# Performance work log

Hardware: AMD Instinct MI355X
Metric: run time of the kernel (lower is better)

Reference implementation:

```python
import jax, jax.numpy as jnp
import numpy as np

NEG_INF = jnp.float32(-(2.0**32) + 1.0)


def squash(z):
    # z: [B, k_max, out_units]
    sq_norm = jnp.sum(jnp.square(z), axis=-1, keepdims=True)
    scale = sq_norm / (1.0 + sq_norm) / jnp.sqrt(sq_norm + 1e-8)
    return scale * z


def setup_inputs() -> dict:
    key = jax.random.key(0)
    k1, k2, k3, k4 = jax.random.split(key, 4)
    B, L, D_IN, D_OUT, K = 1024, 200, 256, 256, 8
    behavior_embeddings = jax.random.normal(k1, (B, L, D_IN), dtype=jnp.float32)
    seq_len = jax.random.randint(k2, (B, 1), 1, L + 1, dtype=jnp.int32)
    routing_logits = jax.random.normal(k3, (1, K, L), dtype=jnp.float32)  # init_std=1.0
    bilinear_mapping_matrix = jax.random.normal(k4, (D_IN, D_OUT), dtype=jnp.float32)
    return {
        "behavior_embeddings": behavior_embeddings,
        "seq_len": seq_len,
        "routing_logits": routing_logits,
        "bilinear_mapping_matrix": bilinear_mapping_matrix,
    }


def reference(behavior_embeddings, seq_len, routing_logits, bilinear_mapping_matrix):
    ITERATION_TIMES = 3
    B, L, _ = behavior_embeddings.shape
    K = routing_logits.shape[1]

    # mask: [B, 1, L] broadcastable to [B, K, L] (same seq_len for every capsule)
    mask = jnp.arange(L)[None, None, :] < seq_len[:, :, None]

    # bilinear map is loop-invariant: [B, L, out_units]
    mapped = jnp.einsum("ble,eo->blo", behavior_embeddings, bilinear_mapping_matrix)

    logits = routing_logits  # [1, K, L]
    interest_capsules = None
    for _ in range(ITERATION_TIMES):
        logits_pad = jnp.where(mask, jnp.broadcast_to(logits, (B, K, L)), NEG_INF)
        weight = jax.nn.softmax(logits_pad, axis=-1)          # [B, K, L]
        Z = jnp.einsum("bkl,blo->bko", weight, mapped)         # [B, K, out]
        interest_capsules = squash(Z)                          # [B, K, out]
        # delta: sum over batch of capsules @ mapped^T -> [1, K, L]
        delta = jnp.einsum("bko,blo->kl", interest_capsules, mapped)[None]
        logits = logits + delta  # emulates assign_add on non-trainable B

    return interest_capsules.reshape(-1, K, interest_capsules.shape[-1])
```

## Files before the change

kernel.cpp:

```cpp
#include <hip/hip_runtime.h>
#include <cstdint>
#include <cstddef>

#define B_    1024
#define L_    200
#define DIN_  256
#define DOUT_ 256
#define K_    8
#define M_    (B_ * L_)

typedef __attribute__((ext_vector_type(8))) short bf16x8;
typedef __attribute__((ext_vector_type(4))) float f32x4;

__device__ __forceinline__ float bf2f(unsigned short u) {
  union { unsigned int i; float f; } w; w.i = ((unsigned int)u) << 16; return w.f;
}
__device__ __forceinline__ unsigned short f2bf(float f) {
  union { float f; unsigned int i; } w; w.f = f;
  unsigned int x = w.i;
  return (unsigned short)((x + 0x7fffu + ((x >> 16) & 1u)) >> 16);
}

__device__ __forceinline__ void gload_lds16(const unsigned short* g, unsigned short* l) {
  __builtin_amdgcn_global_load_lds(
      (const __attribute__((address_space(1))) void*)g,
      (__attribute__((address_space(3))) void*)l, 16, 0, 0);
}

__global__ __launch_bounds__(256)
void wt_prep(const float* __restrict__ W, const float* __restrict__ rlog,
             unsigned short* __restrict__ Wall, float* __restrict__ logitsW)
{
  const int k = blockIdx.x;
  const int n = threadIdx.x;
  const int gi = blockIdx.x * 256 + threadIdx.x;
  if (gi < K_ * L_) logitsW[gi] = rlog[gi];

  float x = W[k * DOUT_ + n];
  unsigned short h = f2bf(x);
  float r = x - bf2f(h);
  unsigned short m = f2bf(r);
  float r2 = r - bf2f(m);
  unsigned short l = f2bf(r2);
  const int k0b = k >> 5, quad = (k >> 3) & 3, j = k & 7;
  const int ntg = n >> 4, lr = n & 15;
  const int lane = quad * 16 + lr;
  Wall[(((size_t)k0b * 3 + 0) * 16 + ntg) * 512 + lane * 8 + j] = h;
  Wall[(((size_t)k0b * 3 + 1) * 16 + ntg) * 512 + lane * 8 + j] = m;
  Wall[(((size_t)k0b * 3 + 2) * 16 + ntg) * 512 + lane * 8 + j] = l;
}

__global__ __launch_bounds__(256, 3)
void gemm_mapped(const float* __restrict__ A,
                 const unsigned short* __restrict__ Wall,
                 float* __restrict__ C)
{
  const int t    = threadIdx.x;
  const int wave = t >> 6;
  const int lane = t & 63;
  const int quad = lane >> 4;
  const int lr   = lane & 15;
  const int m0   = blockIdx.x * 128 + wave * 32;
  const int nt0  = blockIdx.y * 8;

  __shared__ unsigned short Bs[2][24 * 512];

  f32x4 acc[2][8];
  #pragma unroll
  for (int mt = 0; mt < 2; ++mt)
    #pragma unroll
    for (int nt = 0; nt < 8; ++nt)
      acc[mt][nt] = (f32x4){0.f, 0.f, 0.f, 0.f};

  bf16x8 ah[2], am[2], al[2];
  float4 Af[2][2];

#define STAGE(K0B, BUF) do { \
    _Pragma("unroll") \
    for (int _i = 0; _i < 6; ++_i) { \
      const int _c   = wave * 6 + _i; \
      const int _s   = _c >> 3; \
      const int _ntl = _c & 7; \
      const unsigned short* _g = Wall + \
          ((((size_t)(K0B) * 3 + _s) * 16 + nt0 + _ntl) * 512) + lane * 8; \
      gload_lds16(_g, &Bs[BUF][_c * 512]); \
    } \
  } while (0)

  const float* ap0 = A + (size_t)(m0 + lr) * DIN_ + quad * 8;
  const float* ap1 = A + (size_t)(m0 + 16 + lr) * DIN_ + quad * 8;

  STAGE(0, 0);
  Af[0][0] = *(const float4*)(ap0);
  Af[0][1] = *(const float4*)(ap0 + 4);
  Af[1][0] = *(const float4*)(ap1);
  Af[1][1] = *(const float4*)(ap1 + 4);
  __syncthreads();

  for (int k0b = 0; k0b < 8; ++k0b) {
    const int cur = k0b & 1;
    if (k0b < 7) STAGE(k0b + 1, cur ^ 1);

    #pragma unroll
    for (int mt = 0; mt < 2; ++mt) {
      float xs[8] = {Af[mt][0].x, Af[mt][0].y, Af[mt][0].z, Af[mt][0].w,
                     Af[mt][1].x, Af[mt][1].y, Af[mt][1].z, Af[mt][1].w};
      #pragma unroll
      for (int j = 0; j < 8; ++j) {
        unsigned short h = f2bf(xs[j]);
        float r = xs[j] - bf2f(h);
        unsigned short mm = f2bf(r);
        float r2 = r - bf2f(mm);
        unsigned short ll = f2bf(r2);
        ah[mt][j] = (short)h; am[mt][j] = (short)mm; al[mt][j] = (short)ll;
      }
    }
    if (k0b < 7) {
      const int ko = (k0b + 1) * 32;
      Af[0][0] = *(const float4*)(ap0 + ko);
      Af[0][1] = *(const float4*)(ap0 + ko + 4);
      Af[1][0] = *(const float4*)(ap1 + ko);
      Af[1][1] = *(const float4*)(ap1 + ko + 4);
    }

#define GROUP(NT) do { \
    bf16x8 bh = *(const bf16x8*)&Bs[cur][(0 * 8 + (NT)) * 512 + lane * 8]; \
    bf16x8 bm = *(const bf16x8*)&Bs[cur][(1 * 8 + (NT)) * 512 + lane * 8]; \
    bf16x8 bl = *(const bf16x8*)&Bs[cur][(2 * 8 + (NT)) * 512 + lane * 8]; \
    f32x4 c0 = acc[0][NT], c1 = acc[1][NT]; \
    c0 = __builtin_amdgcn_mfma_f32_16x16x32_bf16(ah[0], bh, c0, 0, 0, 0); \
    c1 = __builtin_amdgcn_mfma_f32_16x16x32_bf16(ah[1], bh, c1, 0, 0, 0); \
    c0 = __builtin_amdgcn_mfma_f32_16x16x32_bf16(ah[0], bm, c0, 0, 0, 0); \
    c1 = __builtin_amdgcn_mfma_f32_16x16x32_bf16(ah[1], bm, c1, 0, 0, 0); \
    c0 = __builtin_amdgcn_mfma_f32_16x16x32_bf16(am[0], bh, c0, 0, 0, 0); \
    c1 = __builtin_amdgcn_mfma_f32_16x16x32_bf16(am[1], bh, c1, 0, 0, 0); \
    c0 = __builtin_amdgcn_mfma_f32_16x16x32_bf16(ah[0], bl, c0, 0, 0, 0); \
    c1 = __builtin_amdgcn_mfma_f32_16x16x32_bf16(ah[1], bl, c1, 0, 0, 0); \
    c0 = __builtin_amdgcn_mfma_f32_16x16x32_bf16(am[0], bm, c0, 0, 0, 0); \
    c1 = __builtin_amdgcn_mfma_f32_16x16x32_bf16(am[1], bm, c1, 0, 0, 0); \
    c0 = __builtin_amdgcn_mfma_f32_16x16x32_bf16(al[0], bh, c0, 0, 0, 0); \
    c1 = __builtin_amdgcn_mfma_f32_16x16x32_bf16(al[1], bh, c1, 0, 0, 0); \
    acc[0][NT] = c0; acc[1][NT] = c1; \
  } while (0)

    GROUP(0); GROUP(1); GROUP(2); GROUP(3);
    GROUP(4); GROUP(5); GROUP(6); GROUP(7);
#undef GROUP

    __syncthreads();
  }
#undef STAGE

  #pragma unroll
  for (int mt = 0; mt < 2; ++mt)
    #pragma unroll
    for (int nt = 0; nt < 8; ++nt)
      #pragma unroll
      for (int r = 0; r < 4; ++r) {
        int row = m0 + mt * 16 + quad * 4 + r;
        C[(size_t)row * DOUT_ + (nt0 + nt) * 16 + lr] = acc[mt][nt][r];
      }
}

__global__ __launch_bounds__(256)
void z_kernel(const float* __restrict__ mapped, const float* __restrict__ logits,
              const int* __restrict__ seq_len, float* __restrict__ caps)
{
  const int t    = threadIdx.x;
  const int lane = t & 63;
  const int wave = t >> 6;
  const int b    = blockIdx.x * 4 + wave;
  const int len  = seq_len[b];
  __shared__ float w[4][K_][204];

  #pragma unroll
  for (int k = 0; k < K_; ++k) {
    float v[4];
    float mx = -3.4028235e38f;
    #pragma unroll
    for (int i = 0; i < 4; ++i) {
      int l = lane + 64 * i;
      v[i] = (l < len) ? logits[k * L_ + l] : -3.4028235e38f;
      mx = fmaxf(mx, v[i]);
    }
    #pragma unroll
    for (int s = 1; s < 64; s <<= 1) mx = fmaxf(mx, __shfl_xor(mx, s, 64));
    float e[4]; float sum = 0.f;
    #pragma unroll
    for (int i = 0; i < 4; ++i) {
      int l = lane + 64 * i;
      e[i] = (l < len) ? __expf(v[i] - mx) : 0.f;
      sum += e[i];
    }
    #pragma unroll
    for (int s = 1; s < 64; s <<= 1) sum += __shfl_xor(sum, s, 64);
    float inv = 1.f / sum;
    #pragma unroll
    for (int i = 0; i < 4; ++i) {
      int l = lane + 64 * i;
      if (l < 204) w[wave][k][l] = e[i] * inv;
    }
  }

  f32x4 acc[K_];
  #pragma unroll
  for (int k = 0; k < K_; ++k) acc[k] = (f32x4){0.f, 0.f, 0.f, 0.f};
  const float* mp = mapped + (size_t)b * L_ * DOUT_ + lane * 4;
  const int lceil = (len + 3) & ~3;
  for (int l = 0; l < lceil; l += 4) {
    float4 m0 = *(const float4*)(mp + (size_t)(l + 0) * DOUT_);
    float4 m1 = *(const float4*)(mp + (size_t)(l + 1) * DOUT_);
    float4 m2 = *(const float4*)(mp + (size_t)(l + 2) * DOUT_);
    float4 m3 = *(const float4*)(mp + (size_t)(l + 3) * DOUT_);
    #pragma unroll
    for (int k = 0; k < K_; ++k) {
      float4 wv = *(const float4*)&w[wave][k][l];
      f32x4 c = acc[k];
      c.x += wv.x * m0.x + wv.y * m1.x + wv.z * m2.x + wv.w * m3.x;
      c.y += wv.x * m0.y + wv.y * m1.y + wv.z * m2.y + wv.w * m3.y;
      c.z += wv.x * m0.z + wv.y * m1.z + wv.z * m2.z + wv.w * m3.z;
      c.w += wv.x * m0.w + wv.y * m1.w + wv.z * m2.w + wv.w * m3.w;
      acc[k] = c;
    }
  }

  #pragma unroll
  for (int k = 0; k < K_; ++k) {
    float sq = acc[k].x * acc[k].x + acc[k].y * acc[k].y
             + acc[k].z * acc[k].z + acc[k].w * acc[k].w;
    #pragma unroll
    for (int s = 1; s < 64; s <<= 1) sq += __shfl_xor(sq, s, 64);
    float scale = sq / ((1.f + sq) * sqrtf(sq + 1e-8f));
    float4 o;
    o.x = scale * acc[k].x; o.y = scale * acc[k].y;
    o.z = scale * acc[k].z; o.w = scale * acc[k].w;
    *(float4*)&caps[((size_t)b * K_ + k) * DOUT_ + lane * 4] = o;
  }
}

__global__ __launch_bounds__(256)
void delta_kernel(const float* __restrict__ mapped, const float* __restrict__ caps,
                  float* __restrict__ partials)
{
  const int t    = threadIdx.x;
  const int lane = t & 63;
  const int wave = t >> 6;
  const int lc   = blockIdx.x % 13;
  const int bc   = blockIdx.x / 13;
  const int bsub = (wave >> 1) * 8;
  const int lsub = (wave & 1) * 8;
  const int l0   = lc * 16 + lsub;
  const int b0   = bc * 16 + bsub;
  const int o4   = lane * 4;

  float acc[K_][8];
  #pragma unroll
  for (int k = 0; k < K_; ++k)
    #pragma unroll
    for (int ll = 0; ll < 8; ++ll) acc[k][ll] = 0.f;

  for (int bi = 0; bi < 8; ++bi) {
    const int b = b0 + bi;
    const float* cp = caps + (size_t)b * (K_ * DOUT_) + o4;
    const float* mp = mapped + ((size_t)b * L_ + l0) * DOUT_ + o4;
    float4 cv[K_], mv[8];
    #pragma unroll
    for (int k = 0; k < K_; ++k) cv[k] = *(const float4*)(cp + (size_t)k * DOUT_);
    #pragma unroll
    for (int ll = 0; ll < 8; ++ll) {
      mv[ll] = (l0 + ll < L_) ? *(const float4*)(mp + (size_t)ll * DOUT_)
                              : make_float4(0.f, 0.f, 0.f, 0.f);
    }
    #pragma unroll
    for (int k = 0; k < K_; ++k)
      #pragma unroll
      for (int ll = 0; ll < 8; ++ll)
        acc[k][ll] += cv[k].x * mv[ll].x + cv[k].y * mv[ll].y
                    + cv[k].z * mv[ll].z + cv[k].w * mv[ll].w;
  }

  float out = 0.f;
  #pragma unroll
  for (int k = 0; k < K_; ++k)
    #pragma unroll
    for (int ll = 0; ll < 8; ++ll) {
      float v = acc[k][ll];
      v += __shfl_xor(v, 1, 64);
      v += __shfl_xor(v, 2, 64);
      v += __shfl_xor(v, 4, 64);
      v += __shfl_xor(v, 8, 64);
      v += __shfl_xor(v, 16, 64);
      v += __shfl_xor(v, 32, 64);
      if (lane == k * 8 + ll) out = v;
    }
  __shared__ float red[4][64];
  red[wave][lane] = out;
  __syncthreads();
  if (wave < 2) {
    float v = red[wave][lane] + red[wave + 2][lane];
    const int k  = lane >> 3;
    const int ll = lane & 7;
    const int gl = lc * 16 + wave * 8 + ll;
    if (gl < L_) partials[((size_t)bc * K_ + k) * L_ + gl] = v;
  }
}

__global__ __launch_bounds__(256)
void reduce_kernel(const float* __restrict__ partials, float* __restrict__ logits)
{
  int i = blockIdx.x * 256 + threadIdx.x;
  if (i < K_ * L_) {
    float s = 0.f;
    #pragma unroll 4
    for (int bc = 0; bc < 64; ++bc) s += partials[bc * (K_ * L_) + i];
    logits[i] += s;
  }
}

extern "C" void kernel_launch(void* const* d_in, const int* in_sizes, int n_in,
                              void* d_out, int out_size, void* d_ws, size_t ws_size,
                              hipStream_t stream)
{
  const float* behav = (const float*)d_in[0];
  const int*   slen  = (const int*)d_in[1];
  const float* rlog  = (const float*)d_in[2];
  const float* W     = (const float*)d_in[3];
  float* caps = (float*)d_out;

  char* ws = (char*)d_ws;
  float* logitsW  = (float*)ws;
  float* partials = (float*)(ws + 8192);
  unsigned short* Wall = (unsigned short*)(ws + 458752);
  float* mapped   = (float*)(ws + (1 << 20));

  wt_prep<<<dim3(256), 256, 0, stream>>>(W, rlog, Wall, logitsW);
  gemm_mapped<<<dim3(1600, 2), 256, 0, stream>>>(behav, Wall, mapped);
  for (int it = 0; it < 3; ++it) {
    z_kernel<<<dim3(B_ / 4), 256, 0, stream>>>(mapped, logitsW, slen, caps);
    if (it < 2) {
      delta_kernel<<<dim3(13 * 64), 256, 0, stream>>>(mapped, caps, partials);
      reduce_kernel<<<dim3(7), 256, 0, stream>>>(partials, logitsW);
    }
  }
}
```

Before: 678.6 us.

## Fuse capsule computation and routing delta into one per-batch kernel

Replaces the separate z and delta kernels with a single route kernel that gives each batch element its own 256-thread block. The block first splits the softmax-weighted sum over L across its four waves and combines them in LDS, then reuses the squashed capsules from LDS to compute that batch element's delta over all L positions. The aim is to cut one launch per iteration and to reread `mapped` while it is still cache-resident, instead of streaming it again in a separate kernel. In exchange, per-batch deltas (1024×8×200 floats) are staged in the output buffer, and the 7-block reduce kernel must now serially sum 1024 partials instead of 64. The delta stage also performs a full cross-lane shuffle reduction for every (k, l) pair, which is heavy shuffle work.

```diff
diff --git a/kernel.cpp b/kernel.cpp
--- a/kernel.cpp
+++ b/kernel.cpp
@@ -162,19 +162,22 @@
       }
 }
 
+template <bool FINAL>
 __global__ __launch_bounds__(256)
-void z_kernel(const float* __restrict__ mapped, const float* __restrict__ logits,
-              const int* __restrict__ seq_len, float* __restrict__ caps)
-{
+void route_kernel(const float* __restrict__ mapped, const float* __restrict__ logits,
+                  const int* __restrict__ seq_len, float* __restrict__ out)
+{
+  const int b    = blockIdx.x;
   const int t    = threadIdx.x;
   const int lane = t & 63;
   const int wave = t >> 6;
-  const int b    = blockIdx.x * 4 + wave;
   const int len  = seq_len[b];
-  __shared__ float w[4][K_][204];
-
-  #pragma unroll
-  for (int k = 0; k < K_; ++k) {
+  __shared__ float w[K_][204];
+  __shared__ float red[4][K_][DOUT_];
+
+  #pragma unroll
+  for (int kk = 0; kk < 2; ++kk) {
+    const int k = wave * 2 + kk;
     float v[4];
     float mx = -3.4028235e38f;
     #pragma unroll
@@ -198,23 +201,24 @@
     #pragma unroll
     for (int i = 0; i < 4; ++i) {
       int l = lane + 64 * i;
-      if (l < 204) w[wave][k][l] = e[i] * inv;
-    }
-  }
+      if (l < 204) w[k][l] = e[i] * inv;
+    }
+  }
+  __syncthreads();
 
   f32x4 acc[K_];
   #pragma unroll
   for (int k = 0; k < K_; ++k) acc[k] = (f32x4){0.f, 0.f, 0.f, 0.f};
   const float* mp = mapped + (size_t)b * L_ * DOUT_ + lane * 4;
   const int lceil = (len + 3) & ~3;
-  for (int l = 0; l < lceil; l += 4) {
+  for (int l = wave * 4; l < lceil; l += 16) {
     float4 m0 = *(const float4*)(mp + (size_t)(l + 0) * DOUT_);
     float4 m1 = *(const float4*)(mp + (size_t)(l + 1) * DOUT_);
     float4 m2 = *(const float4*)(mp + (size_t)(l + 2) * DOUT_);
     float4 m3 = *(const float4*)(mp + (size_t)(l + 3) * DOUT_);
     #pragma unroll
     for (int k = 0; k < K_; ++k) {
-      float4 wv = *(const float4*)&w[wave][k][l];
+      float4 wv = *(const float4*)&w[k][l];
       f32x4 c = acc[k];
       c.x += wv.x * m0.x + wv.y * m1.x + wv.z * m2.x + wv.w * m3.x;
       c.y += wv.x * m0.y + wv.y * m1.y + wv.z * m2.y + wv.w * m3.y;
@@ -223,86 +227,71 @@
       acc[k] = c;
     }
   }
-
-  #pragma unroll
-  for (int k = 0; k < K_; ++k) {
-    float sq = acc[k].x * acc[k].x + acc[k].y * acc[k].y
-             + acc[k].z * acc[k].z + acc[k].w * acc[k].w;
+  #pragma unroll
+  for (int k = 0; k < K_; ++k)
+    *(f32x4*)&red[wave][k][lane * 4] = acc[k];
+  __syncthreads();
+
+  #pragma unroll
+  for (int kk = 0; kk < 2; ++kk) {
+    const int k = wave * 2 + kk;
+    float4 s0 = *(const float4*)&red[0][k][lane * 4];
+    float4 s1 = *(const float4*)&red[1][k][lane * 4];
+    float4 s2 = *(const float4*)&red[2][k][lane * 4];
+    float4 s3 = *(const float4*)&red[3][k][lane * 4];
+    float4 z;
+    z.x = (s0.x + s1.x) + (s2.x + s3.x);
+    z.y = (s0.y + s1.y) + (s2.y + s3.y);
+    z.z = (s0.z + s1.z) + (s2.z + s3.z);
+    z.w = (s0.w + s1.w) + (s2.w + s3.w);
+    float sq = z.x * z.x + z.y * z.y + z.z * z.z + z.w * z.w;
     #pragma unroll
     for (int s = 1; s < 64; s <<= 1) sq += __shfl_xor(sq, s, 64);
     float scale = sq / ((1.f + sq) * sqrtf(sq + 1e-8f));
     float4 o;
-    o.x = scale * acc[k].x; o.y = scale * acc[k].y;
-    o.z = scale * acc[k].z; o.w = scale * acc[k].w;
-    *(float4*)&caps[((size_t)b * K_ + k) * DOUT_ + lane * 4] = o;
-  }
-}
-
-__global__ __launch_bounds__(256)
-void delta_kernel(const float* __restrict__ mapped, const float* __restrict__ caps,
-                  float* __restrict__ partials)
-{
-  const int t    = threadIdx.x;
-  const int lane = t & 63;
-  const int wave = t >> 6;
-  const int lc   = blockIdx.x % 13;
-  const int bc   = blockIdx.x / 13;
-  const int bsub = (wave >> 1) * 8;
-  const int lsub = (wave & 1) * 8;
-  const int l0   = lc * 16 + lsub;
-  const int b0   = bc * 16 + bsub;
-  const int o4   = lane * 4;
-
-  float acc[K_][8];
-  #pragma unroll
-  for (int k = 0; k < K_; ++k)
-    #pragma unroll
-    for (int ll = 0; ll < 8; ++ll) acc[k][ll] = 0.f;
-
-  for (int bi = 0; bi < 8; ++bi) {
-    const int b = b0 + bi;
-    const float* cp = caps + (size_t)b * (K_ * DOUT_) + o4;
-    const float* mp = mapped + ((size_t)b * L_ + l0) * DOUT_ + o4;
-    float4 cv[K_], mv[8];
-    #pragma unroll
-    for (int k = 0; k < K_; ++k) cv[k] = *(const float4*)(cp + (size_t)k * DOUT_);
-    #pragma unroll
-    for (int ll = 0; ll < 8; ++ll) {
-      mv[ll] = (l0 + ll < L_) ? *(const float4*)(mp + (size_t)ll * DOUT_)
-                              : make_float4(0.f, 0.f, 0.f, 0.f);
-    }
-    #pragma unroll
-    for (int k = 0; k < K_; ++k)
+    o.x = scale * z.x; o.y = scale * z.y; o.z = scale * z.z; o.w = scale * z.w;
+    if (FINAL) {
+      *(float4*)&out[((size_t)b * K_ + k) * DOUT_ + lane * 4] = o;
+    } else {
+      *(float4*)&red[0][k][lane * 4] = o;
+    }
+  }
+  if (FINAL) return;
+  __syncthreads();
+
+  float* caps_s  = &red[0][0][0];
+  float* delta_s = &red[1][0][0];
+  float4 cv[K_];
+  #pragma unroll
+  for (int k = 0; k < K_; ++k) cv[k] = *(const float4*)&caps_s[k * DOUT_ + lane * 4];
+
+  for (int l0 = wave * 4; l0 < L_; l0 += 16) {
+    float4 m0 = *(const float4*)(mp + (size_t)(l0 + 0) * DOUT_);
+    float4 m1 = *(const float4*)(mp + (size_t)(l0 + 1) * DOUT_);
+    float4 m2 = *(const float4*)(mp + (size_t)(l0 + 2) * DOUT_);
+    float4 m3 = *(const float4*)(mp + (size_t)(l0 + 3) * DOUT_);
+    #pragma unroll
+    for (int k = 0; k < K_; ++k) {
+      float p0 = cv[k].x * m0.x + cv[k].y * m0.y + cv[k].z * m0.z + cv[k].w * m0.w;
+      float p1 = cv[k].x * m1.x + cv[k].y * m1.y + cv[k].z * m1.z + cv[k].w * m1.w;
+      float p2 = cv[k].x * m2.x + cv[k].y * m2.y + cv[k].z * m2.z + cv[k].w * m2.w;
+      float p3 = cv[k].x * m3.x + cv[k].y * m3.y + cv[k].z * m3.z + cv[k].w * m3.w;
       #pragma unroll
-      for (int ll = 0; ll < 8; ++ll)
-        acc[k][ll] += cv[k].x * mv[ll].x + cv[k].y * mv[ll].y
-                    + cv[k].z * mv[ll].z + cv[k].w * mv[ll].w;
-  }
-
-  float out = 0.f;
-  #pragma unroll
-  for (int k = 0; k < K_; ++k)
-    #pragma unroll
-    for (int ll = 0; ll < 8; ++ll) {
-      float v = acc[k][ll];
-      v += __shfl_xor(v, 1, 64);
-      v += __shfl_xor(v, 2, 64);
-      v += __shfl_xor(v, 4, 64);
-      v += __shfl_xor(v, 8, 64);
-      v += __shfl_xor(v, 16, 64);
-      v += __shfl_xor(v, 32, 64);
-      if (lane == k * 8 + ll) out = v;
-    }
-  __shared__ float red[4][64];
-  red[wave][lane] = out;
-  __syncthreads();
-  if (wave < 2) {
-    float v = red[wave][lane] + red[wave + 2][lane];
-    const int k  = lane >> 3;
-    const int ll = lane & 7;
-    const int gl = lc * 16 + wave * 8 + ll;
-    if (gl < L_) partials[((size_t)bc * K_ + k) * L_ + gl] = v;
-  }
+      for (int s = 1; s < 64; s <<= 1) {
+        p0 += __shfl_xor(p0, s, 64);
+        p1 += __shfl_xor(p1, s, 64);
+        p2 += __shfl_xor(p2, s, 64);
+        p3 += __shfl_xor(p3, s, 64);
+      }
+      if (lane == k * 4 + 0) delta_s[k * L_ + l0 + 0] = p0;
+      if (lane == k * 4 + 1) delta_s[k * L_ + l0 + 1] = p1;
+      if (lane == k * 4 + 2) delta_s[k * L_ + l0 + 2] = p2;
+      if (lane == k * 4 + 3) delta_s[k * L_ + l0 + 3] = p3;
+    }
+  }
+  __syncthreads();
+  for (int i = t; i < K_ * L_; i += 256)
+    out[(size_t)b * (K_ * L_) + i] = delta_s[i];
 }
 
 __global__ __launch_bounds__(256)
@@ -311,8 +300,8 @@
   int i = blockIdx.x * 256 + threadIdx.x;
   if (i < K_ * L_) {
     float s = 0.f;
-    #pragma unroll 4
-    for (int bc = 0; bc < 64; ++bc) s += partials[bc * (K_ * L_) + i];
+    #pragma unroll 8
+    for (int b = 0; b < B_; ++b) s += partials[(size_t)b * (K_ * L_) + i];
     logits[i] += s;
   }
 }
@@ -325,21 +314,18 @@
   const int*   slen  = (const int*)d_in[1];
   const float* rlog  = (const float*)d_in[2];
   const float* W     = (const float*)d_in[3];
-  float* caps = (float*)d_out;
+  float* outp = (float*)d_out;
 
   char* ws = (char*)d_ws;
   float* logitsW  = (float*)ws;
-  float* partials = (float*)(ws + 8192);
   unsigned short* Wall = (unsigned short*)(ws + 458752);
   float* mapped   = (float*)(ws + (1 << 20));
 
   wt_prep<<<dim3(256), 256, 0, stream>>>(W, rlog, Wall, logitsW);
   gemm_mapped<<<dim3(1600, 2), 256, 0, stream>>>(behav, Wall, mapped);
-  for (int it = 0; it < 3; ++it) {
-    z_kernel<<<dim3(B_ / 4), 256, 0, stream>>>(mapped, logitsW, slen, caps);
-    if (it < 2) {
-      delta_kernel<<<dim3(13 * 64), 256, 0, stream>>>(mapped, caps, partials);
-      reduce_kernel<<<dim3(7), 256, 0, stream>>>(partials, logitsW);
-    }
-  }
-}
+  for (int it = 0; it < 2; ++it) {
+    route_kernel<false><<<dim3(B_), 256, 0, stream>>>(mapped, logitsW, slen, outp);
+    reduce_kernel<<<dim3(7), 256, 0, stream>>>(outp, logitsW);
+  }
+  route_kernel<true><<<dim3(B_), 256, 0, stream>>>(mapped, logitsW, slen, outp);
+}
```

After: 786.6 us. 1.16x slower.
